# Optimization experiments

Hardware: AMD Instinct MI355X
Metric: run time of the kernel (lower is better)

## Reference

```python
import jax, jax.numpy as jnp
import numpy as np

HID = 128
HEADS = 4
N_LAYERS = 3


def layer_norm(x, g, b, eps=1e-5):
    mu = x.mean(-1, keepdims=True)
    var = ((x - mu) ** 2).mean(-1, keepdims=True)
    return (x - mu) / jnp.sqrt(var + eps) * g + b


def gat_layer(x, W, a_src, a_dst, bias, src, dst):
    # PyG GATConv(hidden, hidden, heads=4, concat=False): mean over heads, +bias
    N = x.shape[0]
    z = (x @ W).reshape(N, HEADS, HID)          # [N, H, D]
    e_src = (z * a_src[None]).sum(-1)           # [N, H]
    e_dst = (z * a_dst[None]).sum(-1)           # [N, H]
    e = jax.nn.leaky_relu(e_src[src] + e_dst[dst], 0.2)  # [E, H]
    m = jax.ops.segment_max(e, dst, num_segments=N)
    p = jnp.exp(e - m[dst])
    s = jax.ops.segment_sum(p, dst, num_segments=N)
    w = p / s[dst]                              # softmax over incoming edges
    out = jax.ops.segment_sum(w[:, :, None] * z[src], dst, num_segments=N)
    return out.mean(1) + bias                   # [N, D]


def _forward(x, node_W, node_b, gat_W, att_src, att_dst, gat_b, ln_g, ln_b,
             sW1, sb1, sW2, sb2, sW3, sb3, edge_index, odd_vertices):
    N = x.shape[0]
    loops = jnp.arange(N)                       # GATConv adds self-loops
    src = jnp.concatenate([edge_index[0], loops])
    dst = jnp.concatenate([edge_index[1], loops])
    h = jax.nn.relu(x @ node_W + node_b)
    for l in range(N_LAYERS):
        hn = gat_layer(h, gat_W[l], att_src[l], att_dst[l], gat_b[l], src, dst)
        hn = layer_norm(hn, ln_g[l], ln_b[l])
        h = jax.nn.relu(hn) + h                 # residual; dropout is eval-mode identity
    emb = h[odd_vertices]                       # [n_odd, D]
    n_odd = emb.shape[0]
    pair = jnp.concatenate([
        jnp.broadcast_to(emb[:, None, :], (n_odd, n_odd, HID)),
        jnp.broadcast_to(emb[None, :, :], (n_odd, n_odd, HID)),
    ], axis=-1)                                 # [n_odd, n_odd, 2D]
    t = jax.nn.relu(pair @ sW1 + sb1)
    t = jax.nn.relu(t @ sW2 + sb2)
    s = (t @ sW3 + sb3)[..., 0]                 # [n_odd, n_odd]
    U = jnp.triu(s, 1)                          # torch fills i<j then mirrors; diag 0
    return U + U.T


def setup_inputs() -> dict:
    key = jax.random.key(0)
    ks = jax.random.split(key, 12)
    N, E, F_IN, N_ODD = 20000, 320000, 5, 512
    sc = 0.05
    inp = {}
    inp["x"] = jax.random.normal(ks[0], (N, F_IN), jnp.float32)
    inp["edge_index"] = jax.random.randint(ks[1], (2, E), 0, N)
    inp["odd_vertices"] = jax.random.randint(ks[2], (N_ODD,), 0, N)
    inp["node_W"] = jax.random.normal(ks[3], (F_IN, HID), jnp.float32) * sc
    inp["node_b"] = jnp.zeros((HID,), jnp.float32)
    inp["gat_W"] = jax.random.normal(ks[4], (N_LAYERS, HID, HEADS * HID), jnp.float32) * sc
    inp["att_src"] = jax.random.normal(ks[5], (N_LAYERS, HEADS, HID), jnp.float32) * sc
    inp["att_dst"] = jax.random.normal(ks[6], (N_LAYERS, HEADS, HID), jnp.float32) * sc
    inp["gat_b"] = jnp.zeros((N_LAYERS, HID), jnp.float32)
    inp["ln_g"] = jnp.ones((N_LAYERS, HID), jnp.float32)
    inp["ln_b"] = jnp.zeros((N_LAYERS, HID), jnp.float32)
    inp["sW1"] = jax.random.normal(ks[7], (2 * HID, HID), jnp.float32) * sc
    inp["sb1"] = jnp.zeros((HID,), jnp.float32)
    inp["sW2"] = jax.random.normal(ks[8], (HID, HID), jnp.float32) * sc
    inp["sb2"] = jnp.zeros((HID,), jnp.float32)
    inp["sW3"] = jax.random.normal(ks[9], (HID, 1), jnp.float32) * sc
    inp["sb3"] = jnp.zeros((1,), jnp.float32)
    return inp


def reference(x, node_W, node_b, gat_W, att_src, att_dst, gat_b, ln_g, ln_b,
              sW1, sb1, sW2, sb2, sW3, sb3, edge_index, odd_vertices):
    return _forward(x, node_W, node_b, gat_W, att_src, att_dst, gat_b, ln_g, ln_b,
                    sW1, sb1, sW2, sb2, sW3, sb3, edge_index, odd_vertices)
```

## Files before the change

kernel.cpp:

```cpp
#include <hip/hip_runtime.h>

#define HID 128
#define HEADS 4
#define NODES 20000
#define NEDGE 320000
#define NTOT (NEDGE + NODES)
#define NODD 512

__global__ void hist_kernel(const int* __restrict__ ei, int* __restrict__ cnt) {
  int e = blockIdx.x * blockDim.x + threadIdx.x;
  if (e >= NTOT) return;
  int d = (e < NEDGE) ? ei[NEDGE + e] : (e - NEDGE);
  atomicAdd(&cnt[d], 1);
}

__global__ void scan_kernel(const int* __restrict__ cnt, int* __restrict__ row_start,
                            int* __restrict__ pos) {
  __shared__ int wsum[16];
  __shared__ int s_carry;
  int t = threadIdx.x;
  int lane = t & 63, wid = t >> 6;
  if (t == 0) s_carry = 0;
  __syncthreads();
  for (int base = 0; base < NODES; base += 1024) {
    int i = base + t;
    int v = (i < NODES) ? cnt[i] : 0;
    int x = v;
    for (int off = 1; off < 64; off <<= 1) {
      int y = __shfl_up(x, off, 64);
      if (lane >= off) x += y;
    }
    if (lane == 63) wsum[wid] = x;
    __syncthreads();
    if (wid == 0) {
      int w = (lane < 16) ? wsum[lane] : 0;
      for (int off = 1; off < 16; off <<= 1) {
        int y = __shfl_up(w, off, 64);
        if (lane >= off) w += y;
      }
      if (lane < 16) wsum[lane] = w;
    }
    __syncthreads();
    int waveoff = (wid == 0) ? 0 : wsum[wid - 1];
    int incl = s_carry + waveoff + x;
    int excl = incl - v;
    if (i < NODES) { row_start[i] = excl; pos[i] = excl; }
    __syncthreads();
    if (t == 1023) s_carry = incl;
    __syncthreads();
  }
  if (t == 0) row_start[NODES] = s_carry;
}

__global__ void scatter_kernel(const int* __restrict__ ei, int* __restrict__ pos,
                               int* __restrict__ csr_src) {
  int e = blockIdx.x * blockDim.x + threadIdx.x;
  if (e >= NTOT) return;
  int s, d;
  if (e < NEDGE) { s = ei[e]; d = ei[NEDGE + e]; } else { s = e - NEDGE; d = s; }
  int p = atomicAdd(&pos[d], 1);
  csr_src[p] = s;
}

__global__ void node_enc_kernel(const float* __restrict__ x, const float* __restrict__ W,
                                const float* __restrict__ b, float* __restrict__ h) {
  int idx = blockIdx.x * blockDim.x + threadIdx.x;
  if (idx >= NODES * HID) return;
  int n = idx >> 7, d = idx & 127;
  const float* xr = x + n * 5;
  float acc = b[d];
#pragma unroll
  for (int k = 0; k < 5; k++) acc = fmaf(xr[k], W[k * HID + d], acc);
  h[idx] = fmaxf(acc, 0.f);
}

__global__ void att_c_kernel(const float* __restrict__ W, const float* __restrict__ a_src,
                             const float* __restrict__ a_dst, float* __restrict__ c_src,
                             float* __restrict__ c_dst) {
  int h = blockIdx.x;
  int k = threadIdx.x;
  const float* wr = W + k * (HEADS * HID) + h * HID;
  const float* as = a_src + h * HID;
  const float* ad = a_dst + h * HID;
  float s1 = 0.f, s2 = 0.f;
  for (int d = 0; d < HID; d++) {
    float w = wr[d];
    s1 = fmaf(w, as[d], s1);
    s2 = fmaf(w, ad[d], s2);
  }
  c_src[h * HID + k] = s1;
  c_dst[h * HID + k] = s2;
}

__global__ __launch_bounds__(256) void e_kernel(const float* __restrict__ h,
    const float* __restrict__ c_src, const float* __restrict__ c_dst,
    float* __restrict__ e_src, float* __restrict__ e_dst) {
  int lane = threadIdx.x & 63;
  int wid = threadIdx.x >> 6;
  int n = blockIdx.x * 4 + wid;
  float v0 = h[n * HID + lane];
  float v1 = h[n * HID + 64 + lane];
#pragma unroll
  for (int hh = 0; hh < HEADS; hh++) {
    float p = v0 * c_src[hh * HID + lane] + v1 * c_src[hh * HID + 64 + lane];
#pragma unroll
    for (int m = 32; m; m >>= 1) p += __shfl_xor(p, m, 64);
    if (lane == 0) e_src[n * HEADS + hh] = p;
    float q = v0 * c_dst[hh * HID + lane] + v1 * c_dst[hh * HID + 64 + lane];
#pragma unroll
    for (int m = 32; m; m >>= 1) q += __shfl_xor(q, m, 64);
    if (lane == 0) e_dst[n * HEADS + hh] = q;
  }
}

__global__ __launch_bounds__(256) void agg_kernel(const float* __restrict__ h,
    const float* __restrict__ e_src, const float* __restrict__ e_dst,
    const int* __restrict__ row_start, const int* __restrict__ csr_src,
    float* __restrict__ agg) {
  __shared__ float4 wsh[4][128];
  __shared__ int ssh[4][128];
  int lane = threadIdx.x & 63;
  int wid = threadIdx.x >> 6;
  int n = blockIdx.x * 4 + wid;
  int r0 = row_start[n], r1 = row_start[n + 1];
  int deg = r1 - r0;
  const float4* es4 = (const float4*)e_src;
  float4 ed = ((const float4*)e_dst)[n];

  int s0 = -1, s1 = -1;
  float4 v0 = {-1e30f, -1e30f, -1e30f, -1e30f};
  float4 v1 = {-1e30f, -1e30f, -1e30f, -1e30f};
  {
    int e = r0 + lane;
    if (e < r1) {
      s0 = csr_src[e];
      float4 es = es4[s0];
      float a = es.x + ed.x, b = es.y + ed.y, c = es.z + ed.z, d = es.w + ed.w;
      v0.x = a > 0.f ? a : 0.2f * a; v0.y = b > 0.f ? b : 0.2f * b;
      v0.z = c > 0.f ? c : 0.2f * c; v0.w = d > 0.f ? d : 0.2f * d;
    }
    e = r0 + 64 + lane;
    if (e < r1) {
      s1 = csr_src[e];
      float4 es = es4[s1];
      float a = es.x + ed.x, b = es.y + ed.y, c = es.z + ed.z, d = es.w + ed.w;
      v1.x = a > 0.f ? a : 0.2f * a; v1.y = b > 0.f ? b : 0.2f * b;
      v1.z = c > 0.f ? c : 0.2f * c; v1.w = d > 0.f ? d : 0.2f * d;
    }
  }
  float4 mx;
  mx.x = fmaxf(v0.x, v1.x); mx.y = fmaxf(v0.y, v1.y);
  mx.z = fmaxf(v0.z, v1.z); mx.w = fmaxf(v0.w, v1.w);
  for (int e = r0 + 128 + lane; e < r1; e += 64) {
    int s = csr_src[e];
    float4 es = es4[s];
    float a = es.x + ed.x, b = es.y + ed.y, c = es.z + ed.z, d = es.w + ed.w;
    mx.x = fmaxf(mx.x, a > 0.f ? a : 0.2f * a);
    mx.y = fmaxf(mx.y, b > 0.f ? b : 0.2f * b);
    mx.z = fmaxf(mx.z, c > 0.f ? c : 0.2f * c);
    mx.w = fmaxf(mx.w, d > 0.f ? d : 0.2f * d);
  }
#pragma unroll
  for (int m = 32; m; m >>= 1) {
    mx.x = fmaxf(mx.x, __shfl_xor(mx.x, m, 64));
    mx.y = fmaxf(mx.y, __shfl_xor(mx.y, m, 64));
    mx.z = fmaxf(mx.z, __shfl_xor(mx.z, m, 64));
    mx.w = fmaxf(mx.w, __shfl_xor(mx.w, m, 64));
  }
  float4 p0 = {0.f, 0.f, 0.f, 0.f}, p1 = {0.f, 0.f, 0.f, 0.f};
  if (s0 >= 0) { p0.x = expf(v0.x - mx.x); p0.y = expf(v0.y - mx.y);
                 p0.z = expf(v0.z - mx.z); p0.w = expf(v0.w - mx.w); }
  if (s1 >= 0) { p1.x = expf(v1.x - mx.x); p1.y = expf(v1.y - mx.y);
                 p1.z = expf(v1.z - mx.z); p1.w = expf(v1.w - mx.w); }
  float4 sm;
  sm.x = p0.x + p1.x; sm.y = p0.y + p1.y; sm.z = p0.z + p1.z; sm.w = p0.w + p1.w;
  for (int e = r0 + 128 + lane; e < r1; e += 64) {
    int s = csr_src[e];
    float4 es = es4[s];
    float a = es.x + ed.x, b = es.y + ed.y, c = es.z + ed.z, d = es.w + ed.w;
    a = a > 0.f ? a : 0.2f * a; b = b > 0.f ? b : 0.2f * b;
    c = c > 0.f ? c : 0.2f * c; d = d > 0.f ? d : 0.2f * d;
    sm.x += expf(a - mx.x); sm.y += expf(b - mx.y);
    sm.z += expf(c - mx.z); sm.w += expf(d - mx.w);
  }
#pragma unroll
  for (int m = 32; m; m >>= 1) {
    sm.x += __shfl_xor(sm.x, m, 64);
    sm.y += __shfl_xor(sm.y, m, 64);
    sm.z += __shfl_xor(sm.z, m, 64);
    sm.w += __shfl_xor(sm.w, m, 64);
  }
  float4 inv;
  inv.x = 1.f / sm.x; inv.y = 1.f / sm.y; inv.z = 1.f / sm.z; inv.w = 1.f / sm.w;

  if (s0 >= 0) {
    float4 w; w.x = p0.x * inv.x; w.y = p0.y * inv.y; w.z = p0.z * inv.z; w.w = p0.w * inv.w;
    wsh[wid][lane] = w; ssh[wid][lane] = s0;
  }
  if (s1 >= 0) {
    float4 w; w.x = p1.x * inv.x; w.y = p1.y * inv.y; w.z = p1.z * inv.z; w.w = p1.w * inv.w;
    wsh[wid][64 + lane] = w; ssh[wid][64 + lane] = s1;
  }
  __builtin_amdgcn_s_waitcnt(0);

  float a00 = 0.f, a01 = 0.f, a10 = 0.f, a11 = 0.f;
  float a20 = 0.f, a21 = 0.f, a30 = 0.f, a31 = 0.f;
  int mcap = deg < 128 ? deg : 128;
  for (int i = 0; i < mcap; i++) {
    float4 w = wsh[wid][i];
    int s = ssh[wid][i];
    float h0 = h[s * HID + lane];
    float h1 = h[s * HID + 64 + lane];
    a00 = fmaf(w.x, h0, a00); a01 = fmaf(w.x, h1, a01);
    a10 = fmaf(w.y, h0, a10); a11 = fmaf(w.y, h1, a11);
    a20 = fmaf(w.z, h0, a20); a21 = fmaf(w.z, h1, a21);
    a30 = fmaf(w.w, h0, a30); a31 = fmaf(w.w, h1, a31);
  }
  for (int e = r0 + 128; e < r1; e++) {
    int s = csr_src[e];
    float4 es = es4[s];
    float a = es.x + ed.x, b = es.y + ed.y, c = es.z + ed.z, d = es.w + ed.w;
    a = a > 0.f ? a : 0.2f * a; b = b > 0.f ? b : 0.2f * b;
    c = c > 0.f ? c : 0.2f * c; d = d > 0.f ? d : 0.2f * d;
    float w0 = expf(a - mx.x) * inv.x, w1 = expf(b - mx.y) * inv.y;
    float w2 = expf(c - mx.z) * inv.z, w3 = expf(d - mx.w) * inv.w;
    float h0 = h[s * HID + lane];
    float h1 = h[s * HID + 64 + lane];
    a00 = fmaf(w0, h0, a00); a01 = fmaf(w0, h1, a01);
    a10 = fmaf(w1, h0, a10); a11 = fmaf(w1, h1, a11);
    a20 = fmaf(w2, h0, a20); a21 = fmaf(w2, h1, a21);
    a30 = fmaf(w3, h0, a30); a31 = fmaf(w3, h1, a31);
  }
  float* ap = agg + n * 512;
  ap[0 * 128 + lane] = a00; ap[0 * 128 + 64 + lane] = a01;
  ap[1 * 128 + lane] = a10; ap[1 * 128 + 64 + lane] = a11;
  ap[2 * 128 + lane] = a20; ap[2 * 128 + 64 + lane] = a21;
  ap[3 * 128 + lane] = a30; ap[3 * 128 + 64 + lane] = a31;
}

__global__ __launch_bounds__(256) void out_ln_kernel(const float* __restrict__ agg,
    const float* __restrict__ W, const float* __restrict__ bias,
    const float* __restrict__ g, const float* __restrict__ b,
    const float* __restrict__ h_in, float* __restrict__ h_out) {
  __shared__ float As[32][36];
  __shared__ float Bs[32][132];
  int tid = threadIdx.x;
  int nb = blockIdx.x * 32;
  int tdim = tid & 31;
  int tnode = tid >> 5;
  float acc[4][4] = {};
  for (int kb = 0; kb < 512; kb += 32) {
    int hh = kb >> 7;
    int kk0 = kb & 127;
    __syncthreads();
    {
      int n = tid >> 3, kq = tid & 7;
      float4 v = *(const float4*)(agg + (nb + n) * 512 + kb + kq * 4);
      As[kq * 4 + 0][n] = v.x; As[kq * 4 + 1][n] = v.y;
      As[kq * 4 + 2][n] = v.z; As[kq * 4 + 3][n] = v.w;
#pragma unroll
      for (int i = 0; i < 4; i++) {
        int idx4 = tid + i * 256;
        int r = idx4 >> 5, dq = idx4 & 31;
        float4 w = *(const float4*)(W + (kk0 + r) * 512 + hh * 128 + dq * 4);
        *(float4*)&Bs[r][dq * 4] = w;
      }
    }
    __syncthreads();
#pragma unroll
    for (int k = 0; k < 32; k++) {
      float4 av = *(const float4*)&As[k][tnode * 4];
      float4 bv = *(const float4*)&Bs[k][tdim * 4];
      acc[0][0] = fmaf(av.x, bv.x, acc[0][0]); acc[0][1] = fmaf(av.x, bv.y, acc[0][1]);
      acc[0][2] = fmaf(av.x, bv.z, acc[0][2]); acc[0][3] = fmaf(av.x, bv.w, acc[0][3]);
      acc[1][0] = fmaf(av.y, bv.x, acc[1][0]); acc[1][1] = fmaf(av.y, bv.y, acc[1][1]);
      acc[1][2] = fmaf(av.y, bv.z, acc[1][2]); acc[1][3] = fmaf(av.y, bv.w, acc[1][3]);
      acc[2][0] = fmaf(av.z, bv.x, acc[2][0]); acc[2][1] = fmaf(av.z, bv.y, acc[2][1]);
      acc[2][2] = fmaf(av.z, bv.z, acc[2][2]); acc[2][3] = fmaf(av.z, bv.w, acc[2][3]);
      acc[3][0] = fmaf(av.w, bv.x, acc[3][0]); acc[3][1] = fmaf(av.w, bv.y, acc[3][1]);
      acc[3][2] = fmaf(av.w, bv.z, acc[3][2]); acc[3][3] = fmaf(av.w, bv.w, acc[3][3]);
    }
  }
  float4 bias4 = *(const float4*)(bias + tdim * 4);
  float4 g4 = *(const float4*)(g + tdim * 4);
  float4 b4 = *(const float4*)(b + tdim * 4);
#pragma unroll
  for (int i = 0; i < 4; i++) {
    int node = nb + tnode * 4 + i;
    float o0 = acc[i][0] * 0.25f + bias4.x;
    float o1 = acc[i][1] * 0.25f + bias4.y;
    float o2 = acc[i][2] * 0.25f + bias4.z;
    float o3 = acc[i][3] * 0.25f + bias4.w;
    float s1 = o0 + o1 + o2 + o3;
    float s2 = o0 * o0 + o1 * o1 + o2 * o2 + o3 * o3;
#pragma unroll
    for (int m = 1; m < 32; m <<= 1) {
      s1 += __shfl_xor(s1, m, 64);
      s2 += __shfl_xor(s2, m, 64);
    }
    float mu = s1 * 0.0078125f;
    float var = s2 * 0.0078125f - mu * mu;
    float r = 1.0f / sqrtf(var + 1e-5f);
    float4 hi = *(const float4*)(h_in + node * 128 + tdim * 4);
    float4 o;
    o.x = fmaxf((o0 - mu) * r * g4.x + b4.x, 0.f) + hi.x;
    o.y = fmaxf((o1 - mu) * r * g4.y + b4.y, 0.f) + hi.y;
    o.z = fmaxf((o2 - mu) * r * g4.z + b4.z, 0.f) + hi.z;
    o.w = fmaxf((o3 - mu) * r * g4.w + b4.w, 0.f) + hi.w;
    *(float4*)(h_out + node * 128 + tdim * 4) = o;
  }
}

__global__ __launch_bounds__(128) void ab_kernel(const float* __restrict__ h,
    const int* __restrict__ odd, const float* __restrict__ sW1,
    const float* __restrict__ sb1, float* __restrict__ As, float* __restrict__ Bs) {
  __shared__ float se[HID];
  int i = blockIdx.x;
  int k = threadIdx.x;
  int node = odd[i];
  se[k] = h[node * HID + k];
  __syncthreads();
  float a = sb1[k], b = 0.f;
  for (int d = 0; d < HID; d++) {
    float e = se[d];
    a = fmaf(e, sW1[d * HID + k], a);
    b = fmaf(e, sW1[(HID + d) * HID + k], b);
  }
  As[i * HID + k] = a;
  Bs[i * HID + k] = b;
}

__global__ __launch_bounds__(256) void score_kernel(const float* __restrict__ As,
    const float* __restrict__ Bs, const float* __restrict__ sW2,
    const float* __restrict__ sb2, const float* __restrict__ sW3,
    const float* __restrict__ sb3, float* __restrict__ out) {
  int i0 = blockIdx.x * 4;
  int j0 = blockIdx.y * 8;
  if (i0 > j0 + 7) return;
  __shared__ float T1[32][36];
  __shared__ float W2s[32][132];
  int tid = threadIdx.x;
  int tn = tid & 31;
  int tp = tid >> 5;
  int sp = tid >> 3;
  int kq = (tid & 7) * 4;
  const float* arow = As + (i0 + (sp >> 3)) * 128;
  const float* brow = Bs + (j0 + (sp & 7)) * 128;
  float acc[4][4] = {};
  for (int kb = 0; kb < 128; kb += 32) {
    __syncthreads();
    {
      float4 a4 = *(const float4*)(arow + kb + kq);
      float4 b4 = *(const float4*)(brow + kb + kq);
      T1[kq + 0][sp] = fmaxf(a4.x + b4.x, 0.f);
      T1[kq + 1][sp] = fmaxf(a4.y + b4.y, 0.f);
      T1[kq + 2][sp] = fmaxf(a4.z + b4.z, 0.f);
      T1[kq + 3][sp] = fmaxf(a4.w + b4.w, 0.f);
#pragma unroll
      for (int i = 0; i < 4; i++) {
        int idx4 = tid + i * 256;
        int r = idx4 >> 5, c = (idx4 & 31) * 4;
        float4 w = *(const float4*)(sW2 + (kb + r) * 128 + c);
        *(float4*)&W2s[r][c] = w;
      }
    }
    __syncthreads();
#pragma unroll
    for (int k = 0; k < 32; k++) {
      float4 av = *(const float4*)&T1[k][tp * 4];
      float4 bv = *(const float4*)&W2s[k][tn * 4];
      acc[0][0] = fmaf(av.x, bv.x, acc[0][0]); acc[0][1] = fmaf(av.x, bv.y, acc[0][1]);
      acc[0][2] = fmaf(av.x, bv.z, acc[0][2]); acc[0][3] = fmaf(av.x, bv.w, acc[0][3]);
      acc[1][0] = fmaf(av.y, bv.x, acc[1][0]); acc[1][1] = fmaf(av.y, bv.y, acc[1][1]);
      acc[1][2] = fmaf(av.y, bv.z, acc[1][2]); acc[1][3] = fmaf(av.y, bv.w, acc[1][3]);
      acc[2][0] = fmaf(av.z, bv.x, acc[2][0]); acc[2][1] = fmaf(av.z, bv.y, acc[2][1]);
      acc[2][2] = fmaf(av.z, bv.z, acc[2][2]); acc[2][3] = fmaf(av.z, bv.w, acc[2][3]);
      acc[3][0] = fmaf(av.w, bv.x, acc[3][0]); acc[3][1] = fmaf(av.w, bv.y, acc[3][1]);
      acc[3][2] = fmaf(av.w, bv.z, acc[3][2]); acc[3][3] = fmaf(av.w, bv.w, acc[3][3]);
    }
  }
  float4 b2v = *(const float4*)(sb2 + tn * 4);
  float4 w3v = *(const float4*)(sW3 + tn * 4);
  float b3v = sb3[0];
#pragma unroll
  for (int pr = 0; pr < 4; pr++) {
    float s = fmaxf(acc[pr][0] + b2v.x, 0.f) * w3v.x
            + fmaxf(acc[pr][1] + b2v.y, 0.f) * w3v.y
            + fmaxf(acc[pr][2] + b2v.z, 0.f) * w3v.z
            + fmaxf(acc[pr][3] + b2v.w, 0.f) * w3v.w;
#pragma unroll
    for (int m = 1; m < 32; m <<= 1) s += __shfl_xor(s, m, 64);
    if (tn == 0) {
      int p = tp * 4 + pr;
      int i = i0 + (p >> 3), j = j0 + (p & 7);
      if (i < j) {
        float v = s + b3v;
        out[i * 512 + j] = v;
        out[j * 512 + i] = v;
      } else if (i == j) {
        out[i * 512 + j] = 0.f;
      }
    }
  }
}

extern "C" void kernel_launch(void* const* d_in, const int* in_sizes, int n_in,
                              void* d_out, int out_size, void* d_ws, size_t ws_size,
                              hipStream_t stream) {
  const float* x       = (const float*)d_in[0];
  const int*   ei      = (const int*)d_in[1];
  const int*   odd     = (const int*)d_in[2];
  const float* node_W  = (const float*)d_in[3];
  const float* node_b  = (const float*)d_in[4];
  const float* gat_W   = (const float*)d_in[5];
  const float* att_src = (const float*)d_in[6];
  const float* att_dst = (const float*)d_in[7];
  const float* gat_b   = (const float*)d_in[8];
  const float* ln_g    = (const float*)d_in[9];
  const float* ln_b    = (const float*)d_in[10];
  const float* sW1     = (const float*)d_in[11];
  const float* sb1     = (const float*)d_in[12];
  const float* sW2     = (const float*)d_in[13];
  const float* sb2     = (const float*)d_in[14];
  const float* sW3     = (const float*)d_in[15];
  const float* sb3     = (const float*)d_in[16];
  float* out = (float*)d_out;

  float* f = (float*)d_ws;
  float* hA  = f; f += NODES * HID;
  float* hB  = f; f += NODES * HID;
  float* agg = f; f += NODES * 512;
  float* e_s = f; f += NODES * 4;
  float* e_d = f; f += NODES * 4;
  float* c_s = f; f += 512;
  float* c_d = f; f += 512;
  float* Asb = f; f += NODD * HID;
  float* Bsb = f; f += NODD * HID;
  int* cnt       = (int*)f;
  int* row_start = cnt + NODES;
  int* pos       = row_start + NODES + 1;
  int* csr       = pos + NODES;

  hipMemsetAsync(cnt, 0, NODES * sizeof(int), stream);
  hist_kernel<<<(NTOT + 255) / 256, 256, 0, stream>>>(ei, cnt);
  scan_kernel<<<1, 1024, 0, stream>>>(cnt, row_start, pos);
  scatter_kernel<<<(NTOT + 255) / 256, 256, 0, stream>>>(ei, pos, csr);
  node_enc_kernel<<<(NODES * HID + 255) / 256, 256, 0, stream>>>(x, node_W, node_b, hA);

  const float* hc = hA;
  float* hn = hB;
  for (int l = 0; l < 3; l++) {
    att_c_kernel<<<HEADS, 128, 0, stream>>>(gat_W + l * HID * 512,
                                            att_src + l * 512, att_dst + l * 512, c_s, c_d);
    e_kernel<<<NODES / 4, 256, 0, stream>>>(hc, c_s, c_d, e_s, e_d);
    agg_kernel<<<NODES / 4, 256, 0, stream>>>(hc, e_s, e_d, row_start, csr, agg);
    out_ln_kernel<<<NODES / 32, 256, 0, stream>>>(agg, gat_W + l * HID * 512,
                                                  gat_b + l * HID, ln_g + l * HID,
                                                  ln_b + l * HID, hc, hn);
    float* t = (float*)hc; hc = hn; hn = t;
  }
  ab_kernel<<<NODD, 128, 0, stream>>>(hc, odd, sW1, sb1, Asb, Bsb);
  score_kernel<<<dim3(128, 64), 256, 0, stream>>>(Asb, Bsb, sW2, sb2, sW3, sb3, out);
}
```

Baseline: 513.6 us.

## Compute last GAT layer only for odd vertices and retile score kernel

The final GAT layer's aggregation and output/LayerNorm now run only for the 512 odd vertices, via an index map, instead of all 20000 nodes. Results are written straight into a compact embedding buffer that ab_kernel reads. This is valid because only h[odd] is consumed downstream, though e_kernel still runs for all nodes since attention scores of every source node are needed. Separately, the score kernel is retiled to 8x8 pair blocks with 8 output columns per thread and a 64x64 grid, which raises register use per thread.

```diff
diff --git a/kernel.cpp b/kernel.cpp
--- a/kernel.cpp
+++ b/kernel.cpp
@@ -116,12 +116,13 @@
 __global__ __launch_bounds__(256) void agg_kernel(const float* __restrict__ h,
     const float* __restrict__ e_src, const float* __restrict__ e_dst,
     const int* __restrict__ row_start, const int* __restrict__ csr_src,
-    float* __restrict__ agg) {
+    float* __restrict__ agg, const int* __restrict__ map) {
   __shared__ float4 wsh[4][128];
   __shared__ int ssh[4][128];
   int lane = threadIdx.x & 63;
   int wid = threadIdx.x >> 6;
-  int n = blockIdx.x * 4 + wid;
+  int idx = blockIdx.x * 4 + wid;
+  int n = map ? map[idx] : idx;
   int r0 = row_start[n], r1 = row_start[n + 1];
   int deg = r1 - r0;
   const float4* es4 = (const float4*)e_src;
@@ -231,7 +232,7 @@
     a20 = fmaf(w2, h0, a20); a21 = fmaf(w2, h1, a21);
     a30 = fmaf(w3, h0, a30); a31 = fmaf(w3, h1, a31);
   }
-  float* ap = agg + n * 512;
+  float* ap = agg + idx * 512;
   ap[0 * 128 + lane] = a00; ap[0 * 128 + 64 + lane] = a01;
   ap[1 * 128 + lane] = a10; ap[1 * 128 + 64 + lane] = a11;
   ap[2 * 128 + lane] = a20; ap[2 * 128 + 64 + lane] = a21;
@@ -241,7 +242,8 @@
 __global__ __launch_bounds__(256) void out_ln_kernel(const float* __restrict__ agg,
     const float* __restrict__ W, const float* __restrict__ bias,
     const float* __restrict__ g, const float* __restrict__ b,
-    const float* __restrict__ h_in, float* __restrict__ h_out) {
+    const float* __restrict__ h_in, float* __restrict__ h_out,
+    const int* __restrict__ map) {
   __shared__ float As[32][36];
   __shared__ float Bs[32][132];
   int tid = threadIdx.x;
@@ -286,7 +288,8 @@
   float4 b4 = *(const float4*)(b + tdim * 4);
 #pragma unroll
   for (int i = 0; i < 4; i++) {
-    int node = nb + tnode * 4 + i;
+    int row = nb + tnode * 4 + i;
+    int res = map ? map[row] : row;
     float o0 = acc[i][0] * 0.25f + bias4.x;
     float o1 = acc[i][1] * 0.25f + bias4.y;
     float o2 = acc[i][2] * 0.25f + bias4.z;
@@ -301,24 +304,23 @@
     float mu = s1 * 0.0078125f;
     float var = s2 * 0.0078125f - mu * mu;
     float r = 1.0f / sqrtf(var + 1e-5f);
-    float4 hi = *(const float4*)(h_in + node * 128 + tdim * 4);
+    float4 hi = *(const float4*)(h_in + res * 128 + tdim * 4);
     float4 o;
     o.x = fmaxf((o0 - mu) * r * g4.x + b4.x, 0.f) + hi.x;
     o.y = fmaxf((o1 - mu) * r * g4.y + b4.y, 0.f) + hi.y;
     o.z = fmaxf((o2 - mu) * r * g4.z + b4.z, 0.f) + hi.z;
     o.w = fmaxf((o3 - mu) * r * g4.w + b4.w, 0.f) + hi.w;
-    *(float4*)(h_out + node * 128 + tdim * 4) = o;
-  }
-}
-
-__global__ __launch_bounds__(128) void ab_kernel(const float* __restrict__ h,
-    const int* __restrict__ odd, const float* __restrict__ sW1,
-    const float* __restrict__ sb1, float* __restrict__ As, float* __restrict__ Bs) {
+    *(float4*)(h_out + row * 128 + tdim * 4) = o;
+  }
+}
+
+__global__ __launch_bounds__(128) void ab_kernel(const float* __restrict__ emb,
+    const float* __restrict__ sW1, const float* __restrict__ sb1,
+    float* __restrict__ As, float* __restrict__ Bs) {
   __shared__ float se[HID];
   int i = blockIdx.x;
   int k = threadIdx.x;
-  int node = odd[i];
-  se[k] = h[node * HID + k];
+  se[k] = emb[i * HID + k];
   __syncthreads();
   float a = sb1[k], b = 0.f;
   for (int d = 0; d < HID; d++) {
@@ -334,28 +336,34 @@
     const float* __restrict__ Bs, const float* __restrict__ sW2,
     const float* __restrict__ sb2, const float* __restrict__ sW3,
     const float* __restrict__ sb3, float* __restrict__ out) {
-  int i0 = blockIdx.x * 4;
-  int j0 = blockIdx.y * 8;
-  if (i0 > j0 + 7) return;
-  __shared__ float T1[32][36];
+  int bx = blockIdx.x, by = blockIdx.y;
+  if (bx > by) return;
+  int i0 = bx * 8, j0 = by * 8;
+  __shared__ float T1[32][68];
   __shared__ float W2s[32][132];
   int tid = threadIdx.x;
-  int tn = tid & 31;
-  int tp = tid >> 5;
-  int sp = tid >> 3;
-  int kq = (tid & 7) * 4;
+  int tn = tid & 15;
+  int tp = tid >> 4;
+  int sp = tid >> 2;
+  int kq = (tid & 3) * 8;
   const float* arow = As + (i0 + (sp >> 3)) * 128;
   const float* brow = Bs + (j0 + (sp & 7)) * 128;
-  float acc[4][4] = {};
+  float acc[4][8] = {};
   for (int kb = 0; kb < 128; kb += 32) {
     __syncthreads();
     {
-      float4 a4 = *(const float4*)(arow + kb + kq);
-      float4 b4 = *(const float4*)(brow + kb + kq);
-      T1[kq + 0][sp] = fmaxf(a4.x + b4.x, 0.f);
-      T1[kq + 1][sp] = fmaxf(a4.y + b4.y, 0.f);
-      T1[kq + 2][sp] = fmaxf(a4.z + b4.z, 0.f);
-      T1[kq + 3][sp] = fmaxf(a4.w + b4.w, 0.f);
+      float4 a0 = *(const float4*)(arow + kb + kq);
+      float4 b0 = *(const float4*)(brow + kb + kq);
+      float4 a1 = *(const float4*)(arow + kb + kq + 4);
+      float4 b1 = *(const float4*)(brow + kb + kq + 4);
+      T1[kq + 0][sp] = fmaxf(a0.x + b0.x, 0.f);
+      T1[kq + 1][sp] = fmaxf(a0.y + b0.y, 0.f);
+      T1[kq + 2][sp] = fmaxf(a0.z + b0.z, 0.f);
+      T1[kq + 3][sp] = fmaxf(a0.w + b0.w, 0.f);
+      T1[kq + 4][sp] = fmaxf(a1.x + b1.x, 0.f);
+      T1[kq + 5][sp] = fmaxf(a1.y + b1.y, 0.f);
+      T1[kq + 6][sp] = fmaxf(a1.z + b1.z, 0.f);
+      T1[kq + 7][sp] = fmaxf(a1.w + b1.w, 0.f);
 #pragma unroll
       for (int i = 0; i < 4; i++) {
         int idx4 = tid + i * 256;
@@ -367,29 +375,36 @@
     __syncthreads();
 #pragma unroll
     for (int k = 0; k < 32; k++) {
-      float4 av = *(const float4*)&T1[k][tp * 4];
-      float4 bv = *(const float4*)&W2s[k][tn * 4];
-      acc[0][0] = fmaf(av.x, bv.x, acc[0][0]); acc[0][1] = fmaf(av.x, bv.y, acc[0][1]);
-      acc[0][2] = fmaf(av.x, bv.z, acc[0][2]); acc[0][3] = fmaf(av.x, bv.w, acc[0][3]);
-      acc[1][0] = fmaf(av.y, bv.x, acc[1][0]); acc[1][1] = fmaf(av.y, bv.y, acc[1][1]);
-      acc[1][2] = fmaf(av.y, bv.z, acc[1][2]); acc[1][3] = fmaf(av.y, bv.w, acc[1][3]);
-      acc[2][0] = fmaf(av.z, bv.x, acc[2][0]); acc[2][1] = fmaf(av.z, bv.y, acc[2][1]);
-      acc[2][2] = fmaf(av.z, bv.z, acc[2][2]); acc[2][3] = fmaf(av.z, bv.w, acc[2][3]);
-      acc[3][0] = fmaf(av.w, bv.x, acc[3][0]); acc[3][1] = fmaf(av.w, bv.y, acc[3][1]);
-      acc[3][2] = fmaf(av.w, bv.z, acc[3][2]); acc[3][3] = fmaf(av.w, bv.w, acc[3][3]);
-    }
-  }
-  float4 b2v = *(const float4*)(sb2 + tn * 4);
-  float4 w3v = *(const float4*)(sW3 + tn * 4);
+      float4 av  = *(const float4*)&T1[k][tp * 4];
+      float4 bv0 = *(const float4*)&W2s[k][tn * 4];
+      float4 bv1 = *(const float4*)&W2s[k][64 + tn * 4];
+#pragma unroll
+      for (int p = 0; p < 4; p++) {
+        float a = (p == 0) ? av.x : (p == 1) ? av.y : (p == 2) ? av.z : av.w;
+        acc[p][0] = fmaf(a, bv0.x, acc[p][0]); acc[p][1] = fmaf(a, bv0.y, acc[p][1]);
+        acc[p][2] = fmaf(a, bv0.z, acc[p][2]); acc[p][3] = fmaf(a, bv0.w, acc[p][3]);
+        acc[p][4] = fmaf(a, bv1.x, acc[p][4]); acc[p][5] = fmaf(a, bv1.y, acc[p][5]);
+        acc[p][6] = fmaf(a, bv1.z, acc[p][6]); acc[p][7] = fmaf(a, bv1.w, acc[p][7]);
+      }
+    }
+  }
+  float4 b2a = *(const float4*)(sb2 + tn * 4);
+  float4 b2b = *(const float4*)(sb2 + 64 + tn * 4);
+  float4 w3a = *(const float4*)(sW3 + tn * 4);
+  float4 w3b = *(const float4*)(sW3 + 64 + tn * 4);
   float b3v = sb3[0];
 #pragma unroll
   for (int pr = 0; pr < 4; pr++) {
-    float s = fmaxf(acc[pr][0] + b2v.x, 0.f) * w3v.x
-            + fmaxf(acc[pr][1] + b2v.y, 0.f) * w3v.y
-            + fmaxf(acc[pr][2] + b2v.z, 0.f) * w3v.z
-            + fmaxf(acc[pr][3] + b2v.w, 0.f) * w3v.w;
-#pragma unroll
-    for (int m = 1; m < 32; m <<= 1) s += __shfl_xor(s, m, 64);
+    float s = fmaxf(acc[pr][0] + b2a.x, 0.f) * w3a.x
+            + fmaxf(acc[pr][1] + b2a.y, 0.f) * w3a.y
+            + fmaxf(acc[pr][2] + b2a.z, 0.f) * w3a.z
+            + fmaxf(acc[pr][3] + b2a.w, 0.f) * w3a.w
+            + fmaxf(acc[pr][4] + b2b.x, 0.f) * w3b.x
+            + fmaxf(acc[pr][5] + b2b.y, 0.f) * w3b.y
+            + fmaxf(acc[pr][6] + b2b.z, 0.f) * w3b.z
+            + fmaxf(acc[pr][7] + b2b.w, 0.f) * w3b.w;
+#pragma unroll
+    for (int m = 1; m < 16; m <<= 1) s += __shfl_xor(s, m, 64);
     if (tn == 0) {
       int p = tp * 4 + pr;
       int i = i0 + (p >> 3), j = j0 + (p & 7);
@@ -436,6 +451,7 @@
   float* c_d = f; f += 512;
   float* Asb = f; f += NODD * HID;
   float* Bsb = f; f += NODD * HID;
+  float* emb = f; f += NODD * HID;
   int* cnt       = (int*)f;
   int* row_start = cnt + NODES;
   int* pos       = row_start + NODES + 1;
@@ -449,16 +465,26 @@
 
   const float* hc = hA;
   float* hn = hB;
-  for (int l = 0; l < 3; l++) {
+  for (int l = 0; l < 2; l++) {
     att_c_kernel<<<HEADS, 128, 0, stream>>>(gat_W + l * HID * 512,
                                             att_src + l * 512, att_dst + l * 512, c_s, c_d);
     e_kernel<<<NODES / 4, 256, 0, stream>>>(hc, c_s, c_d, e_s, e_d);
-    agg_kernel<<<NODES / 4, 256, 0, stream>>>(hc, e_s, e_d, row_start, csr, agg);
+    agg_kernel<<<NODES / 4, 256, 0, stream>>>(hc, e_s, e_d, row_start, csr, agg, nullptr);
     out_ln_kernel<<<NODES / 32, 256, 0, stream>>>(agg, gat_W + l * HID * 512,
                                                   gat_b + l * HID, ln_g + l * HID,
-                                                  ln_b + l * HID, hc, hn);
+                                                  ln_b + l * HID, hc, hn, nullptr);
     float* t = (float*)hc; hc = hn; hn = t;
   }
-  ab_kernel<<<NODD, 128, 0, stream>>>(hc, odd, sW1, sb1, Asb, Bsb);
-  score_kernel<<<dim3(128, 64), 256, 0, stream>>>(Asb, Bsb, sW2, sb2, sW3, sb3, out);
-}
+  {
+    const int l = 2;
+    att_c_kernel<<<HEADS, 128, 0, stream>>>(gat_W + l * HID * 512,
+                                            att_src + l * 512, att_dst + l * 512, c_s, c_d);
+    e_kernel<<<NODES / 4, 256, 0, stream>>>(hc, c_s, c_d, e_s, e_d);
+    agg_kernel<<<NODD / 4, 256, 0, stream>>>(hc, e_s, e_d, row_start, csr, agg, odd);
+    out_ln_kernel<<<NODD / 32, 256, 0, stream>>>(agg, gat_W + l * HID * 512,
+                                                 gat_b + l * HID, ln_g + l * HID,
+                                                 ln_b + l * HID, hc, emb, odd);
+  }
+  ab_kernel<<<NODD, 128, 0, stream>>>(emb, sW1, sb1, Asb, Bsb);
+  score_kernel<<<dim3(64, 64), 256, 0, stream>>>(Asb, Bsb, sW2, sb2, sW3, sb3, out);
+}
```

Result: faster. 465.3 us (-9.4%).
